# Optimization experiments

Measured on AMD Instinct MI355X. Metric: run time of the kernel, lower is better.

## Reference

```python
import jax, jax.numpy as jnp
import numpy as np

SQRT_HALF = np.float32(np.sqrt(0.5))


def _weight_norm(v, g):
    # torch weight_norm dim=0: per-output-row normalization, w = g * v / ||v||_row
    return (g / jnp.linalg.norm(v, axis=1))[:, None] * v


def setup_inputs() -> dict:
    key = jax.random.key(0)
    ks = jax.random.split(key, 6)
    B, L, C, E, H, W = 32, 1024, 1024, 1024, 14, 14
    return {
        "x": jax.random.normal(ks[0], (B, L, C), dtype=jnp.float32),
        "word_embed": jax.random.normal(ks[1], (B, L, E), dtype=jnp.float32),
        "conv_feats": jax.random.normal(ks[2], (B, E, H, W), dtype=jnp.float32),
        "in_v": jax.random.normal(ks[3], (E, C), dtype=jnp.float32) * np.float32(1.0 / np.sqrt(C)),
        "in_g": jnp.ones((E,), dtype=jnp.float32),
        "in_b": jnp.zeros((E,), dtype=jnp.float32),
        "out_v": jax.random.normal(ks[4], (C, E), dtype=jnp.float32) * np.float32(1.0 / np.sqrt(E)),
        "out_g": jnp.ones((C,), dtype=jnp.float32),
        "out_b": jnp.zeros((C,), dtype=jnp.float32),
    }


def reference(x, word_embed, conv_feats, in_v, in_g, in_b, out_v, out_g, out_b):
    # in_projection (weight-normed linear) + word_embed, scaled
    Wi = _weight_norm(in_v, in_g)                      # [E, C]
    h = (jnp.einsum('blc,ec->ble', x, Wi) + in_b + word_embed) * SQRT_HALF  # [B, L, E]

    B, E, H, W = conv_feats.shape
    n = H * W
    y = conv_feats.reshape(B, E, n)                    # [B, E, n]
    scores = jnp.einsum('ble,bev->blv', h, y)          # [B, L, n]
    attn = jax.nn.softmax(scores, axis=-1)             # [B, L, n]
    ctx = jnp.einsum('blv,bev->ble', attn, y)          # [B, L, E]
    ctx = ctx * jnp.asarray(n * np.sqrt(1.0 / n), dtype=ctx.dtype)  # = sqrt(n)

    # out_projection + residual, scaled
    Wo = _weight_norm(out_v, out_g)                    # [C, E]
    out = (jnp.einsum('ble,ce->blc', ctx, Wo) + out_b + x) * SQRT_HALF  # [B, L, C]
    return out, attn
```

## Files before the change

kernel.cpp:

```cpp
#include <hip/hip_runtime.h>
#include <hip/hip_bf16.h>

typedef unsigned short u16;
typedef _Float16 f16x8 __attribute__((ext_vector_type(8)));
typedef unsigned short u16x8 __attribute__((ext_vector_type(8)));
typedef float f32x4 __attribute__((ext_vector_type(4)));

#define SQHF 0.70710678118654752440f

__device__ __forceinline__ u16 f2h(float f) {
  const _Float16 h = (_Float16)f;
  return __builtin_bit_cast(u16, h);
}

template <int N>
__device__ __forceinline__ void vmwait() {
  asm volatile("s_waitcnt vmcnt(%0)" ::"i"(N) : "memory");
}

__device__ __forceinline__ void gload_lds16(const void* g, void* l) {
  __builtin_amdgcn_global_load_lds(
      (const __attribute__((address_space(1))) unsigned int*)g,
      (__attribute__((address_space(3))) unsigned int*)l, 16, 0, 0);
}

__device__ __forceinline__ float block_sum(float v) {
#pragma unroll
  for (int o = 32; o; o >>= 1) v += __shfl_xor(v, o);
  __shared__ float red[4];
  if ((threadIdx.x & 63) == 0) red[threadIdx.x >> 6] = v;
  __syncthreads();
  return red[0] + red[1] + red[2] + red[3];
}

__global__ void wnorm_t_kernel(const float* __restrict__ v, const float* __restrict__ g,
                               u16* __restrict__ wtf) {
  const int e = blockIdx.x;
  const float* vr = v + (long)e * 1024;
  float ss = 0.f;
  for (int c = threadIdx.x; c < 1024; c += 256) { float t = vr[c]; ss += t * t; }
  const float tot = block_sum(ss);
  const float scl = g[e] / sqrtf(tot);
  for (int c = threadIdx.x; c < 1024; c += 256) wtf[(long)c * 1024 + e] = f2h(vr[c] * scl);
}

__global__ void wnorm_kernel(const float* __restrict__ v, const float* __restrict__ g,
                             u16* __restrict__ w) {
  const int c = blockIdx.x;
  const float* vr = v + (long)c * 1024;
  float ss = 0.f;
  for (int e = threadIdx.x; e < 1024; e += 256) { float t = vr[e]; ss += t * t; }
  const float tot = block_sum(ss);
  const float scl = g[c] / sqrtf(tot);
  for (int e = threadIdx.x; e < 1024; e += 256) w[(long)c * 1024 + e] = f2h(vr[e] * scl);
}

__global__ void prep_y_kernel(const float* __restrict__ conv, const float* __restrict__ in_b,
                              u16* __restrict__ concat, float* __restrict__ rc) {
  const int b = blockIdx.x >> 4;
  const int e0 = (blockIdx.x & 15) << 6;
  __shared__ float tile[64 * 224];
  const float* cb = conv + ((long)b * 1024 + e0) * 196;
  for (int idx = threadIdx.x; idx < 64 * 224; idx += 256) {
    const int rr = idx / 224, vv = idx - rr * 224;
    tile[idx] = (vv < 196) ? cb[(long)rr * 196 + vv] : 0.f;
  }
  __syncthreads();
  for (int idx = threadIdx.x; idx < 256 * 64; idx += 256) {
    const int vr = idx >> 6, c = idx & 63;
    const float val = (vr < 224) ? tile[c * 224 + vr] : 0.f;
    concat[((long)b * 256 + vr) * 2048 + 1024 + e0 + c] = f2h(val);
  }
  const int v = threadIdx.x;
  if (v < 196) {
    float s = 0.f;
#pragma unroll 8
    for (int rr = 0; rr < 64; ++rr) s += in_b[e0 + rr] * tile[rr * 224 + v];
    atomicAdd(&rc[b * 256 + v], s);
  }
}

__global__ void softmax_kernel(const float* __restrict__ s0b, const float* __restrict__ s1b,
                               const float* __restrict__ rc,
                               float* __restrict__ attn, u16* __restrict__ attn_f) {
  const long row = (long)blockIdx.x * 4 + (threadIdx.x >> 6);
  const int lane = threadIdx.x & 63;
  const int b = (int)(row >> 10);
  const float* s0 = s0b + row * 256;
  const float* s1 = s1b + row * 256;
  const float* rcb = rc + b * 256;
  float v0 = (s0[lane] + s1[lane] + rcb[lane]) * SQHF;
  float v1 = (s0[64 + lane] + s1[64 + lane] + rcb[64 + lane]) * SQHF;
  float v2 = (s0[128 + lane] + s1[128 + lane] + rcb[128 + lane]) * SQHF;
  float v3 = (lane < 4) ? (s0[192 + lane] + s1[192 + lane] + rcb[192 + lane]) * SQHF : -1e30f;
  float mx = fmaxf(fmaxf(v0, v1), fmaxf(v2, v3));
#pragma unroll
  for (int o = 32; o; o >>= 1) mx = fmaxf(mx, __shfl_xor(mx, o));
  const float e0 = __expf(v0 - mx), e1 = __expf(v1 - mx), e2 = __expf(v2 - mx);
  const float e3 = (lane < 4) ? __expf(v3 - mx) : 0.f;
  float sm = e0 + e1 + e2 + e3;
#pragma unroll
  for (int o = 32; o; o >>= 1) sm += __shfl_xor(sm, o);
  const float inv = 1.f / sm;
  float* arow = attn + row * 196;
  arow[lane] = e0 * inv;
  arow[64 + lane] = e1 * inv;
  arow[128 + lane] = e2 * inv;
  if (lane < 4) arow[192 + lane] = e3 * inv;
  u16* brow = attn_f + row * 256;
  brow[lane] = f2h(e0 * inv);
  brow[64 + lane] = f2h(e1 * inv);
  brow[128 + lane] = f2h(e2 * inv);
  brow[192 + lane] = (lane < 4) ? f2h(e3 * inv) : (u16)0;
}

__global__ __launch_bounds__(512) void gemm_scores(
    const float* __restrict__ Af0, const float* __restrict__ Af1,
    const u16* __restrict__ Bh, long bStride,
    float* __restrict__ out0, float* __restrict__ out1) {
  constexpr int TBH = 8192;
  constexpr int HSM = 16384;
  __shared__ __align__(16) u16 smem[HSM * 2];

  int bid = blockIdx.x;
  const int half = bid & 1;
  bid >>= 1;
  const int nwg = gridDim.x >> 1;
  const int q = nwg >> 3, xcd = bid & 7, l8 = bid >> 3;
  const int mTile = xcd * q + l8;
  const long rowBase = (long)mTile << 8;
  const int kOff = half << 10;

  const long bOff = (long)(mTile >> 2) * bStride;
  const u16* Bg = Bh + bOff;

  const int tid = threadIdx.x;
  const int wave = tid >> 6, lane = tid & 63;
  const int wr = wave >> 2, wc = wave & 3;
  const int lr = lane & 15;

  const int sbr = tid >> 2;
  const int sbc = tid & 3;
  const int arow = tid >> 1, akch = tid & 1;
  const int aswz = (arow >> 1) & 3;
  const int aoff0 = arow * 32 + ((akch ^ aswz) << 3);
  const int aoff1 = arow * 32 + (((akch + 2) ^ aswz) << 3);

  f32x4 acc[8][4];
#pragma unroll
  for (int m = 0; m < 8; ++m)
#pragma unroll
    for (int n = 0; n < 4; ++n) acc[m][n] = f32x4{0.f, 0.f, 0.f, 0.f};

  f32x4 ra0, ra1, rb0, rb1;
  auto issueA = [&](int k0) {
    const int gk = k0 + kOff;
    const float* As = (gk < 1024) ? (Af0 + rowBase * 1024 + gk)
                                  : (Af1 + rowBase * 1024 + (gk - 1024));
    const float* p = As + (long)arow * 1024 + akch * 8;
    ra0 = *(const f32x4*)p;        ra1 = *(const f32x4*)(p + 4);
    rb0 = *(const f32x4*)(p + 16); rb1 = *(const f32x4*)(p + 20);
  };
  auto writeA = [&](int buf) {
    u16* sb = smem + buf * HSM;
    u16x8 w0, w1;
    w0[0] = f2h(ra0[0]); w0[1] = f2h(ra0[1]); w0[2] = f2h(ra0[2]); w0[3] = f2h(ra0[3]);
    w0[4] = f2h(ra1[0]); w0[5] = f2h(ra1[1]); w0[6] = f2h(ra1[2]); w0[7] = f2h(ra1[3]);
    w1[0] = f2h(rb0[0]); w1[1] = f2h(rb0[1]); w1[2] = f2h(rb0[2]); w1[3] = f2h(rb0[3]);
    w1[4] = f2h(rb1[0]); w1[5] = f2h(rb1[1]); w1[6] = f2h(rb1[2]); w1[7] = f2h(rb1[3]);
    *(u16x8*)&sb[aoff0] = w0;
    *(u16x8*)&sb[aoff1] = w1;
  };
  auto stageB = [&](int buf, int k0) {
    u16* sb = smem + buf * HSM;
#pragma unroll
    for (int i = 0; i < 2; ++i) {
      const int row = i * 128 + sbr;
      const int csw = ((sbc ^ ((row >> 1) & 3)) << 3);
      gload_lds16(Bg + (long)row * 2048 + k0 + kOff + csw,
                  &smem[buf * HSM + TBH + i * 4096 + wave * 512]);
      (void)sb;
    }
  };

  auto compute = [&](int buf) {
    const u16* sb = smem + buf * HSM;
    f16x8 fb[4];
#pragma unroll
    for (int n = 0; n < 4; ++n) {
      const int row = wc * 64 + n * 16 + lr;
      const int off = TBH + row * 32 + (((lane >> 4) ^ ((row >> 1) & 3)) << 3);
      fb[n] = __builtin_bit_cast(f16x8, *(const u16x8*)&sb[off]);
    }
#pragma unroll
    for (int h = 0; h < 2; ++h) {
      f16x8 fa[4];
#pragma unroll
      for (int m = 0; m < 4; ++m) {
        const int row = wr * 128 + (h * 4 + m) * 16 + lr;
        const int off = row * 32 + (((lane >> 4) ^ ((row >> 1) & 3)) << 3);
        fa[m] = __builtin_bit_cast(f16x8, *(const u16x8*)&sb[off]);
      }
      __builtin_amdgcn_s_setprio(1);
#pragma unroll
      for (int m = 0; m < 4; ++m)
#pragma unroll
        for (int n = 0; n < 4; ++n)
          acc[h * 4 + m][n] =
              __builtin_amdgcn_mfma_f32_16x16x32_f16(fa[m], fb[n], acc[h * 4 + m][n], 0, 0, 0);
      __builtin_amdgcn_s_setprio(0);
    }
  };

  const int nSteps = 32;
  issueA(0); stageB(0, 0);
  vmwait<2>();
  writeA(0);
  issueA(32); stageB(1, 32);
  for (int t = 0; t < nSteps; ++t) {
    if (t + 1 < nSteps) {
      asm volatile("s_waitcnt vmcnt(6) lgkmcnt(0)" ::: "memory");
    } else {
      asm volatile("s_waitcnt vmcnt(0) lgkmcnt(0)" ::: "memory");
    }
    __builtin_amdgcn_s_barrier();
    __builtin_amdgcn_sched_barrier(0);
    compute(t & 1);
    __builtin_amdgcn_sched_barrier(0);
    __builtin_amdgcn_s_barrier();
    if (t + 1 < nSteps) {
      vmwait<2>();
      writeA((t + 1) & 1);
      if (t + 2 < nSteps) { issueA((t + 2) << 5); stageB(t & 1, (t + 2) << 5); }
    }
  }

  float* o = half ? out1 : out0;
  const int rloc = (lane >> 4) << 2;
#pragma unroll
  for (int m = 0; m < 8; ++m) {
#pragma unroll
    for (int n = 0; n < 4; ++n) {
      const int col = wc * 64 + n * 16 + lr;
#pragma unroll
      for (int j = 0; j < 4; ++j) {
        const long row = rowBase + wr * 128 + m * 16 + rloc + j;
        o[row * 256 + col] = acc[m][n][j];
      }
    }
  }
}

template <int EPI>
__global__ __launch_bounds__(256) void gemm128(
    const u16* __restrict__ Ah, const u16* __restrict__ Bh,
    int N, int K, int ldA, int ldB, int ldOut,
    int mTilesPerBatch, long bStride, int aTilesMod,
    const float* __restrict__ bias, const float* __restrict__ extra,
    float scale, void* __restrict__ out1) {
  constexpr int TBH = 4096;
  constexpr int HSM = 8192;
  __shared__ __align__(16) u16 smem[HSM * 2];

  const int bid = blockIdx.x, nwg = gridDim.x;
  const int numN = N >> 7;
  const int q = nwg >> 3, r = nwg & 7, xcd = bid & 7, l8 = bid >> 3;
  const int wg = (xcd < r ? xcd * (q + 1) : r * (q + 1) + (xcd - r) * q) + l8;
  const int mTile = wg / numN, nTile = wg - mTile * numN;
  const long rowBase = (long)mTile << 7;
  const int colBase = nTile << 7;
  const int aTile = aTilesMod ? (mTile % aTilesMod) : mTile;
  const long aRowBase = (long)aTile << 7;
  const long bOff = mTilesPerBatch ? (long)(mTile / mTilesPerBatch) * bStride : 0;

  const u16* Agh = Ah + aRowBase * ldA;
  const u16* Bgh = Bh + bOff + (long)colBase * ldB;

  const int tid = threadIdx.x;
  const int wave = tid >> 6, lane = tid & 63;
  const int wr = wave >> 1, wc = wave & 1;
  const int sr = wave * 16 + (lane >> 2);
  const int scS = (((lane & 3) ^ ((sr >> 1) & 3)) << 3);
  const int lr = lane & 15;

  f32x4 acc[4][4];
#pragma unroll
  for (int m = 0; m < 4; ++m)
#pragma unroll
    for (int n = 0; n < 4; ++n) acc[m][n] = f32x4{0.f, 0.f, 0.f, 0.f};

  auto stage = [&](int buf, int k0) {
    u16* sb = smem + buf * HSM;
#pragma unroll
    for (int i = 0; i < 2; ++i) {
      const long roA = (long)(i * 64 + sr) * ldA + k0 + scS;
      const long roB = (long)(i * 64 + sr) * ldB + k0 + scS;
      const int lo_ = i * 2048 + wave * 512;
      gload_lds16(Agh + roA, &sb[lo_]);
      gload_lds16(Bgh + roB, &sb[TBH + lo_]);
    }
  };

  auto compute = [&](int buf) {
    const u16* sb = smem + buf * HSM;
    f16x8 fa[4], fb[4];
#pragma unroll
    for (int m = 0; m < 4; ++m) {
      const int row = wr * 64 + m * 16 + lr;
      const int off = row * 32 + (((lane >> 4) ^ ((row >> 1) & 3)) << 3);
      fa[m] = __builtin_bit_cast(f16x8, *(const u16x8*)&sb[off]);
    }
#pragma unroll
    for (int n = 0; n < 4; ++n) {
      const int row = wc * 64 + n * 16 + lr;
      const int off = row * 32 + (((lane >> 4) ^ ((row >> 1) & 3)) << 3);
      fb[n] = __builtin_bit_cast(f16x8, *(const u16x8*)&sb[TBH + off]);
    }
    __builtin_amdgcn_s_setprio(1);
#pragma unroll
    for (int m = 0; m < 4; ++m)
#pragma unroll
      for (int n = 0; n < 4; ++n)
        acc[m][n] = __builtin_amdgcn_mfma_f32_16x16x32_f16(fa[m], fb[n], acc[m][n], 0, 0, 0);
    __builtin_amdgcn_s_setprio(0);
  };

  const int nSteps = K >> 5;
  stage(0, 0);
  for (int t = 0; t < nSteps; ++t) {
    const int cur = t & 1;
    if (t + 1 < nSteps) {
      stage(cur ^ 1, (t + 1) << 5);
      vmwait<4>();
    } else {
      vmwait<0>();
    }
    __builtin_amdgcn_s_barrier();
    __builtin_amdgcn_sched_barrier(0);
    compute(cur);
    __builtin_amdgcn_sched_barrier(0);
    __builtin_amdgcn_s_barrier();
  }

  const int rloc = (lane >> 4) << 2;
#pragma unroll
  for (int m = 0; m < 4; ++m) {
#pragma unroll
    for (int n = 0; n < 4; ++n) {
      const int col = colBase + wc * 64 + n * 16 + lr;
#pragma unroll
      for (int j = 0; j < 4; ++j) {
        const long row = rowBase + wr * 64 + m * 16 + rloc + j;
        const float v = acc[m][n][j];
        if (EPI == 1) {
          ((float*)out1)[row * (long)ldOut + col] =
              (v + bias[col] + extra[row * (long)ldOut + col]) * scale;
        } else if (EPI == 6) {
          ((u16*)out1)[row * (long)ldOut + col] = f2h(v * scale);
        }
      }
    }
  }
}

extern "C" void kernel_launch(void* const* d_in, const int* in_sizes, int n_in,
                              void* d_out, int out_size, void* d_ws, size_t ws_size,
                              hipStream_t stream) {
  (void)in_sizes; (void)n_in; (void)out_size; (void)ws_size;
  const float* x     = (const float*)d_in[0];
  const float* we    = (const float*)d_in[1];
  const float* conv  = (const float*)d_in[2];
  const float* in_v  = (const float*)d_in[3];
  const float* in_g  = (const float*)d_in[4];
  const float* in_b  = (const float*)d_in[5];
  const float* out_v = (const float*)d_in[6];
  const float* out_g = (const float*)d_in[7];
  const float* out_b = (const float*)d_in[8];
  float* out  = (float*)d_out;
  float* attn = out + 33554432l;

  char* ws = (char*)d_ws;
  u16* concat = (u16*)(ws);
  u16* wtf    = (u16*)(ws + 33554432l);
  u16* wo     = (u16*)(ws + 35651584l);
  u16* zo     = (u16*)(ws + 37748736l);
  u16* attf   = (u16*)(ws + 54525952l);
  float* rc   = (float*)(ws + 71303168l);
  float* s1   = (float*)(ws + 71368704l);
  float* s0   = out;

  hipMemsetAsync(rc, 0, 32 * 256 * sizeof(float), stream);
  wnorm_t_kernel<<<1024, 256, 0, stream>>>(in_v, in_g, wtf);
  wnorm_kernel<<<1024, 256, 0, stream>>>(out_v, out_g, wo);
  prep_y_kernel<<<512, 256, 0, stream>>>(conv, in_b, concat, rc);
  gemm128<6><<<512, 256, 0, stream>>>(
      concat + 1024, wtf, 1024, 1024, 2048, 1024, 2048,
      0, 0, 0, nullptr, nullptr, 1.f, concat);
  gemm_scores<<<256, 512, 0, stream>>>(x, we, concat, 524288l, s0, s1);
  softmax_kernel<<<8192, 256, 0, stream>>>(s0, s1, rc, attn, attf);
  gemm128<6><<<512, 256, 0, stream>>>(
      wo, concat + 1024, 256, 1024, 1024, 2048, 256,
      8, 524288l, 8, nullptr, nullptr, 14.f, zo);
  gemm128<1><<<2048, 256, 0, stream>>>(
      attf, zo, 1024, 256, 256, 256, 1024,
      8, 262144l, 0, out_b, x, SQHF, out);
}
```

Measured before the change: 290.8 us.

## Load fp32 A fragments straight into registers in scores GEMM, drop LDS staging

Rewrites the scores GEMM so each wave loads its own fp32 rows of x or word_embed directly into registers and converts them to fp16 MFMA fragments, instead of staging A through LDS. Only the B tile (256 columns) is staged in LDS via direct global-to-LDS loads. Tiles shrink to 128 rows with 256-thread blocks and twice as many blocks, and each half-block picks x or word_embed up front rather than branching per k-step. The goal is to remove the LDS write/read traffic and a barrier-guarded copy stage for A. In exchange each wave holds more accumulators, there is less cross-wave reuse of A, and global loads are less coalesced.

```diff
diff --git a/kernel.cpp b/kernel.cpp
--- a/kernel.cpp
+++ b/kernel.cpp
@@ -114,12 +114,11 @@
   brow[192 + lane] = (lane < 4) ? f2h(e3 * inv) : (u16)0;
 }
 
-__global__ __launch_bounds__(512) void gemm_scores(
-    const float* __restrict__ Af0, const float* __restrict__ Af1,
-    const u16* __restrict__ Bh, long bStride,
+__global__ __launch_bounds__(256) void gemm_scores2(
+    const float* __restrict__ x, const float* __restrict__ we,
+    const u16* __restrict__ Bh,
     float* __restrict__ out0, float* __restrict__ out1) {
-  constexpr int TBH = 8192;
-  constexpr int HSM = 16384;
+  constexpr int HSM = 8192;
   __shared__ __align__(16) u16 smem[HSM * 2];
 
   int bid = blockIdx.x;
@@ -128,127 +127,114 @@
   const int nwg = gridDim.x >> 1;
   const int q = nwg >> 3, xcd = bid & 7, l8 = bid >> 3;
   const int mTile = xcd * q + l8;
-  const long rowBase = (long)mTile << 8;
+  const long rowBase = (long)mTile << 7;
   const int kOff = half << 10;
 
-  const long bOff = (long)(mTile >> 2) * bStride;
-  const u16* Bg = Bh + bOff;
+  const u16* Bg = Bh + (long)(mTile >> 3) * 524288l;
+  const float* Ab = half ? we : x;
 
   const int tid = threadIdx.x;
   const int wave = tid >> 6, lane = tid & 63;
-  const int wr = wave >> 2, wc = wave & 3;
   const int lr = lane & 15;
-
-  const int sbr = tid >> 2;
-  const int sbc = tid & 3;
-  const int arow = tid >> 1, akch = tid & 1;
-  const int aswz = (arow >> 1) & 3;
-  const int aoff0 = arow * 32 + ((akch ^ aswz) << 3);
-  const int aoff1 = arow * 32 + (((akch + 2) ^ aswz) << 3);
-
-  f32x4 acc[8][4];
-#pragma unroll
-  for (int m = 0; m < 8; ++m)
-#pragma unroll
-    for (int n = 0; n < 4; ++n) acc[m][n] = f32x4{0.f, 0.f, 0.f, 0.f};
-
-  f32x4 ra0, ra1, rb0, rb1;
-  auto issueA = [&](int k0) {
-    const int gk = k0 + kOff;
-    const float* As = (gk < 1024) ? (Af0 + rowBase * 1024 + gk)
-                                  : (Af1 + rowBase * 1024 + (gk - 1024));
-    const float* p = As + (long)arow * 1024 + akch * 8;
-    ra0 = *(const f32x4*)p;        ra1 = *(const f32x4*)(p + 4);
-    rb0 = *(const f32x4*)(p + 16); rb1 = *(const f32x4*)(p + 20);
-  };
-  auto writeA = [&](int buf) {
-    u16* sb = smem + buf * HSM;
-    u16x8 w0, w1;
-    w0[0] = f2h(ra0[0]); w0[1] = f2h(ra0[1]); w0[2] = f2h(ra0[2]); w0[3] = f2h(ra0[3]);
-    w0[4] = f2h(ra1[0]); w0[5] = f2h(ra1[1]); w0[6] = f2h(ra1[2]); w0[7] = f2h(ra1[3]);
-    w1[0] = f2h(rb0[0]); w1[1] = f2h(rb0[1]); w1[2] = f2h(rb0[2]); w1[3] = f2h(rb0[3]);
-    w1[4] = f2h(rb1[0]); w1[5] = f2h(rb1[1]); w1[6] = f2h(rb1[2]); w1[7] = f2h(rb1[3]);
-    *(u16x8*)&sb[aoff0] = w0;
-    *(u16x8*)&sb[aoff1] = w1;
-  };
+  const int lk8 = (lane >> 4) << 3;
+
+  const float* Ar0 = Ab + (rowBase + wave * 32 + lr) * 1024l + lk8;
+  const float* Ar1 = Ar0 + 16 * 1024l;
+
+  const int sr_ = lane >> 2;
+  const int sc_ = lane & 3;
+
+  f32x4 acc[2][16];
+#pragma unroll
+  for (int m = 0; m < 2; ++m)
+#pragma unroll
+    for (int n = 0; n < 16; ++n) acc[m][n] = f32x4{0.f, 0.f, 0.f, 0.f};
+
+  f32x4 aE0, aE1, aE2, aE3, aO0, aO1, aO2, aO3;
+
   auto stageB = [&](int buf, int k0) {
     u16* sb = smem + buf * HSM;
 #pragma unroll
-    for (int i = 0; i < 2; ++i) {
-      const int row = i * 128 + sbr;
-      const int csw = ((sbc ^ ((row >> 1) & 3)) << 3);
-      gload_lds16(Bg + (long)row * 2048 + k0 + kOff + csw,
-                  &smem[buf * HSM + TBH + i * 4096 + wave * 512]);
-      (void)sb;
-    }
-  };
-
-  auto compute = [&](int buf) {
+    for (int i = 0; i < 4; ++i) {
+      const int r = i * 64 + wave * 16 + sr_;
+      const int csw = ((sc_ ^ ((r >> 1) & 3)) << 3);
+      gload_lds16(Bg + (long)r * 2048 + k0 + kOff + csw,
+                  &sb[(i * 256 + wave * 64) * 8]);
+    }
+  };
+  auto issueE = [&](int k0) {
+    const float* p0 = Ar0 + k0;
+    const float* p1 = Ar1 + k0;
+    aE0 = *(const f32x4*)p0; aE1 = *(const f32x4*)(p0 + 4);
+    aE2 = *(const f32x4*)p1; aE3 = *(const f32x4*)(p1 + 4);
+  };
+  auto issueO = [&](int k0) {
+    const float* p0 = Ar0 + k0;
+    const float* p1 = Ar1 + k0;
+    aO0 = *(const f32x4*)p0; aO1 = *(const f32x4*)(p0 + 4);
+    aO2 = *(const f32x4*)p1; aO3 = *(const f32x4*)(p1 + 4);
+  };
+
+  auto computeS = [&](int buf, const f32x4& a0, const f32x4& a1,
+                      const f32x4& a2, const f32x4& a3) {
     const u16* sb = smem + buf * HSM;
-    f16x8 fb[4];
-#pragma unroll
-    for (int n = 0; n < 4; ++n) {
-      const int row = wc * 64 + n * 16 + lr;
-      const int off = TBH + row * 32 + (((lane >> 4) ^ ((row >> 1) & 3)) << 3);
-      fb[n] = __builtin_bit_cast(f16x8, *(const u16x8*)&sb[off]);
-    }
-#pragma unroll
-    for (int h = 0; h < 2; ++h) {
-      f16x8 fa[4];
-#pragma unroll
-      for (int m = 0; m < 4; ++m) {
-        const int row = wr * 128 + (h * 4 + m) * 16 + lr;
-        const int off = row * 32 + (((lane >> 4) ^ ((row >> 1) & 3)) << 3);
-        fa[m] = __builtin_bit_cast(f16x8, *(const u16x8*)&sb[off]);
-      }
-      __builtin_amdgcn_s_setprio(1);
-#pragma unroll
-      for (int m = 0; m < 4; ++m)
-#pragma unroll
-        for (int n = 0; n < 4; ++n)
-          acc[h * 4 + m][n] =
-              __builtin_amdgcn_mfma_f32_16x16x32_f16(fa[m], fb[n], acc[h * 4 + m][n], 0, 0, 0);
-      __builtin_amdgcn_s_setprio(0);
-    }
-  };
-
-  const int nSteps = 32;
-  issueA(0); stageB(0, 0);
-  vmwait<2>();
-  writeA(0);
-  issueA(32); stageB(1, 32);
-  for (int t = 0; t < nSteps; ++t) {
-    if (t + 1 < nSteps) {
-      asm volatile("s_waitcnt vmcnt(6) lgkmcnt(0)" ::: "memory");
+    f16x8 fa0, fa1;
+    fa0[0] = (_Float16)a0[0]; fa0[1] = (_Float16)a0[1];
+    fa0[2] = (_Float16)a0[2]; fa0[3] = (_Float16)a0[3];
+    fa0[4] = (_Float16)a1[0]; fa0[5] = (_Float16)a1[1];
+    fa0[6] = (_Float16)a1[2]; fa0[7] = (_Float16)a1[3];
+    fa1[0] = (_Float16)a2[0]; fa1[1] = (_Float16)a2[1];
+    fa1[2] = (_Float16)a2[2]; fa1[3] = (_Float16)a2[3];
+    fa1[4] = (_Float16)a3[0]; fa1[5] = (_Float16)a3[1];
+    fa1[6] = (_Float16)a3[2]; fa1[7] = (_Float16)a3[3];
+    __builtin_amdgcn_s_setprio(1);
+#pragma unroll
+    for (int n = 0; n < 16; ++n) {
+      const int v = n * 16 + lr;
+      const int off = v * 32 + (((lane >> 4) ^ ((v >> 1) & 3)) << 3);
+      const f16x8 fb = __builtin_bit_cast(f16x8, *(const u16x8*)&sb[off]);
+      acc[0][n] = __builtin_amdgcn_mfma_f32_16x16x32_f16(fa0, fb, acc[0][n], 0, 0, 0);
+      acc[1][n] = __builtin_amdgcn_mfma_f32_16x16x32_f16(fa1, fb, acc[1][n], 0, 0, 0);
+    }
+    __builtin_amdgcn_s_setprio(0);
+  };
+
+  issueE(0);
+  stageB(0, 0);
+  for (int t = 0; t < 32; t += 2) {
+    issueO((t + 1) << 5);
+    stageB(1, (t + 1) << 5);
+    vmwait<8>();
+    __builtin_amdgcn_s_barrier();
+    __builtin_amdgcn_sched_barrier(0);
+    computeS(0, aE0, aE1, aE2, aE3);
+    __builtin_amdgcn_sched_barrier(0);
+    __builtin_amdgcn_s_barrier();
+    if (t + 2 < 32) {
+      issueE((t + 2) << 5);
+      stageB(0, (t + 2) << 5);
+      vmwait<8>();
     } else {
-      asm volatile("s_waitcnt vmcnt(0) lgkmcnt(0)" ::: "memory");
-    }
-    __builtin_amdgcn_s_barrier();
-    __builtin_amdgcn_sched_barrier(0);
-    compute(t & 1);
-    __builtin_amdgcn_sched_barrier(0);
-    __builtin_amdgcn_s_barrier();
-    if (t + 1 < nSteps) {
-      vmwait<2>();
-      writeA((t + 1) & 1);
-      if (t + 2 < nSteps) { issueA((t + 2) << 5); stageB(t & 1, (t + 2) << 5); }
-    }
+      vmwait<0>();
+    }
+    __builtin_amdgcn_s_barrier();
+    __builtin_amdgcn_sched_barrier(0);
+    computeS(1, aO0, aO1, aO2, aO3);
+    __builtin_amdgcn_sched_barrier(0);
+    __builtin_amdgcn_s_barrier();
   }
 
   float* o = half ? out1 : out0;
   const int rloc = (lane >> 4) << 2;
 #pragma unroll
-  for (int m = 0; m < 8; ++m) {
-#pragma unroll
-    for (int n = 0; n < 4; ++n) {
-      const int col = wc * 64 + n * 16 + lr;
+  for (int m = 0; m < 2; ++m)
+#pragma unroll
+    for (int n = 0; n < 16; ++n)
 #pragma unroll
       for (int j = 0; j < 4; ++j) {
-        const long row = rowBase + wr * 128 + m * 16 + rloc + j;
-        o[row * 256 + col] = acc[m][n][j];
+        const long row = rowBase + wave * 32 + m * 16 + rloc + j;
+        o[row * 256 + n * 16 + lr] = acc[m][n][j];
       }
-    }
-  }
 }
 
 template <int EPI>
@@ -396,7 +382,7 @@
   gemm128<6><<<512, 256, 0, stream>>>(
       concat + 1024, wtf, 1024, 1024, 2048, 1024, 2048,
       0, 0, 0, nullptr, nullptr, 1.f, concat);
-  gemm_scores<<<256, 512, 0, stream>>>(x, we, concat, 524288l, s0, s1);
+  gemm_scores2<<<512, 256, 0, stream>>>(x, we, concat, s0, s1);
   softmax_kernel<<<8192, 256, 0, stream>>>(s0, s1, rc, attn, attf);
   gemm128<6><<<512, 256, 0, stream>>>(
       wo, concat + 1024, 256, 1024, 1024, 2048, 256,
```

After: 314.8 us. 1.08x slower.

## Retile scores GEMM to 128x128 tiles with direct fp32 LDS staging

Applied to the files above, without the earlier changes.

Rewrites the scores GEMM to use 128x128 output tiles with 4 waves and 1024 blocks, in place of 256x256 tiles with 8 waves and 256 blocks. The fp32 A operand (x / word_embed) is now copied straight to LDS with async global-to-LDS loads and converted to fp16 when the fragments are read, instead of passing through registers and being converted before the LDS write. This is meant to drop the register staging and improve occupancy and load balance across CUs. In exchange the fp32 A tile doubles LDS traffic per element, and the smaller tiles mean more B reloads and less reuse per block.

```diff
diff --git a/kernel.cpp b/kernel.cpp
--- a/kernel.cpp
+++ b/kernel.cpp
@@ -114,12 +114,12 @@
   brow[192 + lane] = (lane < 4) ? f2h(e3 * inv) : (u16)0;
 }
 
-__global__ __launch_bounds__(512) void gemm_scores(
-    const float* __restrict__ Af0, const float* __restrict__ Af1,
-    const u16* __restrict__ Bh, long bStride,
+__global__ __launch_bounds__(256) void gemm_scores_r8(
+    const float* __restrict__ x, const float* __restrict__ we,
+    const u16* __restrict__ Bh,
     float* __restrict__ out0, float* __restrict__ out1) {
   constexpr int TBH = 8192;
-  constexpr int HSM = 16384;
+  constexpr int HSM = 12288;
   __shared__ __align__(16) u16 smem[HSM * 2];
 
   int bid = blockIdx.x;
@@ -127,128 +127,109 @@
   bid >>= 1;
   const int nwg = gridDim.x >> 1;
   const int q = nwg >> 3, xcd = bid & 7, l8 = bid >> 3;
-  const int mTile = xcd * q + l8;
-  const long rowBase = (long)mTile << 8;
+  const int wg = xcd * q + l8;
+  const int mTile = wg >> 1, nTile = wg & 1;
+  const long rowBase = (long)mTile << 7;
+  const int colBase = nTile << 7;
   const int kOff = half << 10;
 
-  const long bOff = (long)(mTile >> 2) * bStride;
-  const u16* Bg = Bh + bOff;
+  const float* Ab = half ? we : x;
+  const float* Ag = Ab + rowBase * 1024;
+  const u16* Bg = Bh + (long)(mTile >> 3) * 524288l + (long)colBase * 2048;
 
   const int tid = threadIdx.x;
   const int wave = tid >> 6, lane = tid & 63;
-  const int wr = wave >> 2, wc = wave & 3;
+  const int wr = wave >> 1, wc = wave & 1;
+  const int sr = wave * 16 + (lane >> 2);
+  const int scS = (((lane & 3) ^ ((sr >> 1) & 3)) << 3);
   const int lr = lane & 15;
-
-  const int sbr = tid >> 2;
-  const int sbc = tid & 3;
-  const int arow = tid >> 1, akch = tid & 1;
-  const int aswz = (arow >> 1) & 3;
-  const int aoff0 = arow * 32 + ((akch ^ aswz) << 3);
-  const int aoff1 = arow * 32 + (((akch + 2) ^ aswz) << 3);
-
-  f32x4 acc[8][4];
-#pragma unroll
-  for (int m = 0; m < 8; ++m)
+  const int lk = (lane >> 4) << 3;
+
+  f32x4 acc[4][4];
+#pragma unroll
+  for (int m = 0; m < 4; ++m)
 #pragma unroll
     for (int n = 0; n < 4; ++n) acc[m][n] = f32x4{0.f, 0.f, 0.f, 0.f};
 
-  f32x4 ra0, ra1, rb0, rb1;
-  auto issueA = [&](int k0) {
-    const int gk = k0 + kOff;
-    const float* As = (gk < 1024) ? (Af0 + rowBase * 1024 + gk)
-                                  : (Af1 + rowBase * 1024 + (gk - 1024));
-    const float* p = As + (long)arow * 1024 + akch * 8;
-    ra0 = *(const f32x4*)p;        ra1 = *(const f32x4*)(p + 4);
-    rb0 = *(const f32x4*)(p + 16); rb1 = *(const f32x4*)(p + 20);
-  };
-  auto writeA = [&](int buf) {
+  auto stage = [&](int buf, int k0) {
     u16* sb = smem + buf * HSM;
-    u16x8 w0, w1;
-    w0[0] = f2h(ra0[0]); w0[1] = f2h(ra0[1]); w0[2] = f2h(ra0[2]); w0[3] = f2h(ra0[3]);
-    w0[4] = f2h(ra1[0]); w0[5] = f2h(ra1[1]); w0[6] = f2h(ra1[2]); w0[7] = f2h(ra1[3]);
-    w1[0] = f2h(rb0[0]); w1[1] = f2h(rb0[1]); w1[2] = f2h(rb0[2]); w1[3] = f2h(rb0[3]);
-    w1[4] = f2h(rb1[0]); w1[5] = f2h(rb1[1]); w1[6] = f2h(rb1[2]); w1[7] = f2h(rb1[3]);
-    *(u16x8*)&sb[aoff0] = w0;
-    *(u16x8*)&sb[aoff1] = w1;
-  };
-  auto stageB = [&](int buf, int k0) {
-    u16* sb = smem + buf * HSM;
+    const float* As = Ag + k0;
+    const int rr = tid >> 3;
+#pragma unroll
+    for (int i = 0; i < 4; ++i) {
+      const int row = i * 32 + rr;
+      const int csw = (((tid & 7) ^ (row & 7)) << 2);
+      gload_lds16(As + (long)row * 1024 + csw, &sb[i * 2048 + wave * 512]);
+    }
 #pragma unroll
     for (int i = 0; i < 2; ++i) {
-      const int row = i * 128 + sbr;
-      const int csw = ((sbc ^ ((row >> 1) & 3)) << 3);
-      gload_lds16(Bg + (long)row * 2048 + k0 + kOff + csw,
-                  &smem[buf * HSM + TBH + i * 4096 + wave * 512]);
-      (void)sb;
+      const long ro = (long)(i * 64 + sr) * 2048 + k0 + kOff + scS;
+      gload_lds16(Bg + ro, &sb[TBH + i * 2048 + wave * 512]);
     }
   };
 
   auto compute = [&](int buf) {
     const u16* sb = smem + buf * HSM;
-    f16x8 fb[4];
+    f16x8 fa[4], fb[4];
+    const char* smemb = (const char*)sb;
+#pragma unroll
+    for (int m = 0; m < 4; ++m) {
+      const int row = wr * 64 + m * 16 + lr;
+      const int xr = (row & 7) << 4;
+      const char* rp = smemb + row * 128;
+      const f32x4 p0 = *(const f32x4*)(rp + ((lk << 2) ^ xr));
+      const f32x4 p1 = *(const f32x4*)(rp + (((lk << 2) + 16) ^ xr));
+      f16x8 va;
+      va[0] = (_Float16)p0.x; va[1] = (_Float16)p0.y;
+      va[2] = (_Float16)p0.z; va[3] = (_Float16)p0.w;
+      va[4] = (_Float16)p1.x; va[5] = (_Float16)p1.y;
+      va[6] = (_Float16)p1.z; va[7] = (_Float16)p1.w;
+      fa[m] = va;
+    }
 #pragma unroll
     for (int n = 0; n < 4; ++n) {
       const int row = wc * 64 + n * 16 + lr;
       const int off = TBH + row * 32 + (((lane >> 4) ^ ((row >> 1) & 3)) << 3);
       fb[n] = __builtin_bit_cast(f16x8, *(const u16x8*)&sb[off]);
     }
-#pragma unroll
-    for (int h = 0; h < 2; ++h) {
-      f16x8 fa[4];
-#pragma unroll
-      for (int m = 0; m < 4; ++m) {
-        const int row = wr * 128 + (h * 4 + m) * 16 + lr;
-        const int off = row * 32 + (((lane >> 4) ^ ((row >> 1) & 3)) << 3);
-        fa[m] = __builtin_bit_cast(f16x8, *(const u16x8*)&sb[off]);
-      }
-      __builtin_amdgcn_s_setprio(1);
-#pragma unroll
-      for (int m = 0; m < 4; ++m)
-#pragma unroll
-        for (int n = 0; n < 4; ++n)
-          acc[h * 4 + m][n] =
-              __builtin_amdgcn_mfma_f32_16x16x32_f16(fa[m], fb[n], acc[h * 4 + m][n], 0, 0, 0);
-      __builtin_amdgcn_s_setprio(0);
-    }
+    __builtin_amdgcn_s_setprio(1);
+#pragma unroll
+    for (int m = 0; m < 4; ++m)
+#pragma unroll
+      for (int n = 0; n < 4; ++n)
+        acc[m][n] = __builtin_amdgcn_mfma_f32_16x16x32_f16(fa[m], fb[n], acc[m][n], 0, 0, 0);
+    __builtin_amdgcn_s_setprio(0);
   };
 
-  const int nSteps = 32;
-  issueA(0); stageB(0, 0);
-  vmwait<2>();
-  writeA(0);
-  issueA(32); stageB(1, 32);
-  for (int t = 0; t < nSteps; ++t) {
-    if (t + 1 < nSteps) {
-      asm volatile("s_waitcnt vmcnt(6) lgkmcnt(0)" ::: "memory");
+  stage(0, 0);
+  for (int t = 0; t < 32; ++t) {
+    const int cur = t & 1;
+    if (t + 1 < 32) {
+      stage(cur ^ 1, (t + 1) << 5);
+      vmwait<6>();
     } else {
-      asm volatile("s_waitcnt vmcnt(0) lgkmcnt(0)" ::: "memory");
+      vmwait<0>();
     }
     __builtin_amdgcn_s_barrier();
     __builtin_amdgcn_sched_barrier(0);
-    compute(t & 1);
+    compute(cur);
     __builtin_amdgcn_sched_barrier(0);
     __builtin_amdgcn_s_barrier();
-    if (t + 1 < nSteps) {
-      vmwait<2>();
-      writeA((t + 1) & 1);
-      if (t + 2 < nSteps) { issueA((t + 2) << 5); stageB(t & 1, (t + 2) << 5); }
-    }
   }
 
   float* o = half ? out1 : out0;
   const int rloc = (lane >> 4) << 2;
 #pragma unroll
-  for (int m = 0; m < 8; ++m) {
+  for (int m = 0; m < 4; ++m)
 #pragma unroll
     for (int n = 0; n < 4; ++n) {
-      const int col = wc * 64 + n * 16 + lr;
+      const int col = colBase + wc * 64 + n * 16 + lr;
 #pragma unroll
       for (int j = 0; j < 4; ++j) {
-        const long row = rowBase + wr * 128 + m * 16 + rloc + j;
+        const long row = rowBase + wr * 64 + m * 16 + rloc + j;
         o[row * 256 + col] = acc[m][n][j];
       }
     }
-  }
 }
 
 template <int EPI>
@@ -396,7 +377,7 @@
   gemm128<6><<<512, 256, 0, stream>>>(
       concat + 1024, wtf, 1024, 1024, 2048, 1024, 2048,
       0, 0, 0, nullptr, nullptr, 1.f, concat);
-  gemm_scores<<<256, 512, 0, stream>>>(x, we, concat, 524288l, s0, s1);
+  gemm_scores_r8<<<1024, 256, 0, stream>>>(x, we, concat, s0, s1);
   softmax_kernel<<<8192, 256, 0, stream>>>(s0, s1, rc, attn, attf);
   gemm128<6><<<512, 256, 0, stream>>>(
       wo, concat + 1024, 256, 1024, 1024, 2048, 256,
```

Measured after the change: 305.4 us. 1.05x slower.
